# Kernel tuning notes

Measured on AMD Instinct MI355X. Metric: run time of the kernel, lower is better.

Reference implementation:

```python
import jax, jax.numpy as jnp
import numpy as np

ANGSTROM2BOHR = 1.8897261258369282
CUTOFF_ANGSTROM = 5.2  # module's `cutoff` init arg, converted to bohr in forward


def smooth_cutoff(d, rc):
    # torchani 'smooth' cutoff: exp(1 - 1/(1 - (d/rc)^2)) for d < rc, else 0
    x2 = (d / rc) ** 2
    x2_safe = jnp.where(x2 < 1.0, x2, 0.0)  # avoid inf inside the masked branch
    return jnp.where(d < rc, jnp.exp(1.0 - 1.0 / (1.0 - x2_safe)), 0.0)


def setup_inputs() -> dict:
    key = jax.random.key(0)
    k0, k1, k2, k3 = jax.random.split(key, 4)
    n_mol, n_atoms, n_pairs = 4096, 64, 16 * 1024 * 1024
    n_elem = 4  # H, C, N, O
    species = jax.random.randint(k0, (n_mol, n_atoms), 0, n_elem)
    energies = jnp.zeros((n_mol,), jnp.float32)
    atom_index12 = jax.random.randint(k1, (2, n_pairs), 0, n_mol * n_atoms)
    distances = jax.random.uniform(k2, (n_pairs,), jnp.float32, 0.5, 6.0)  # angstrom
    # exp_prefactor = -scaling_charge * sqrt(outer(Z, Z)) / 2, Z = [1, 6, 7, 8]
    z = jnp.array([1.0, 6.0, 7.0, 8.0], jnp.float32)
    exp_prefactor = (-0.016 * jnp.sqrt(jnp.outer(z, z)) / 2.0).astype(jnp.float32)
    # distances_factor = -scaling_radius / cutoff_radii (symmetric pairwise radii table)
    radii = jax.random.uniform(k3, (n_elem, n_elem), jnp.float32, 2.0, 5.0)
    radii = 0.5 * (radii + radii.T)
    distances_factor = (-10.0 / radii).astype(jnp.float32)
    return {
        "species": species,
        "energies": energies,
        "atom_index12": atom_index12,
        "distances": distances,
        "exp_prefactor": exp_prefactor,
        "distances_factor": distances_factor,
    }


def reference(species, energies, atom_index12, distances, exp_prefactor, distances_factor):
    n_mol, n_atoms = species.shape
    d = distances * ANGSTROM2BOHR  # [P]
    species12 = species.reshape(-1)[atom_index12]  # [2, P] gather
    pre = exp_prefactor[species12[0], species12[1]]   # [P]
    dfac = distances_factor[species12[0], species12[1]]  # [P]
    srb = pre * jnp.exp(dfac * d)
    srb = srb * smooth_cutoff(d, CUTOFF_ANGSTROM * ANGSTROM2BOHR)
    mol_idx = atom_index12[0] // n_atoms  # [P]
    out = energies + jax.ops.segment_sum(srb, mol_idx, num_segments=n_mol)
    return species, out
```

## Files before the change

kernel.cpp:

```cpp
#include <hip/hip_runtime.h>
#include <math.h>


__global__ void pack_species_kernel(const int* __restrict__ sp,
                                    unsigned* __restrict__ packed, int nwords) {
    int w = blockIdx.x * blockDim.x + threadIdx.x;
    if (w >= nwords) return;
    const int4* p4 = (const int4*)(sp + (w << 4));
    int4 a = p4[0], b = p4[1], c = p4[2], d = p4[3];
    unsigned v =
        (unsigned)(a.x & 3)        | ((unsigned)(a.y & 3) << 2)  |
        ((unsigned)(a.z & 3) << 4) | ((unsigned)(a.w & 3) << 6)  |
        ((unsigned)(b.x & 3) << 8) | ((unsigned)(b.y & 3) << 10) |
        ((unsigned)(b.z & 3) << 12)| ((unsigned)(b.w & 3) << 14) |
        ((unsigned)(c.x & 3) << 16)| ((unsigned)(c.y & 3) << 18) |
        ((unsigned)(c.z & 3) << 20)| ((unsigned)(c.w & 3) << 22) |
        ((unsigned)(d.x & 3) << 24)| ((unsigned)(d.y & 3) << 26) |
        ((unsigned)(d.z & 3) << 28)| ((unsigned)(d.w & 3) << 30);
    packed[w] = v;
}

__global__ void init_out_kernel(const int* __restrict__ species,
                                const float* __restrict__ energies,
                                float* __restrict__ out,
                                int n_species, int n_mol) {
    int i = blockIdx.x * blockDim.x + threadIdx.x;
    if (i < n_species) {
        out[i] = (float)species[i];
    } else if (i < n_species + n_mol) {
        out[i] = energies[i - n_species];
    }
}

template <bool FROM_WS>
__global__ __launch_bounds__(1024, 1)
void srb_main_kernel(const unsigned* __restrict__ packed_ws,
                     const int* __restrict__ species,
                     const int* __restrict__ ai,
                     const float* __restrict__ dist,
                     const float* __restrict__ pre_tab,
                     const float* __restrict__ dfac_tab,
                     float* __restrict__ out_e,
                     int P, int mol_shift) {
    __shared__ unsigned packed[16384];
    __shared__ float bins[4096];
    __shared__ float2 tab[16];

    const int t  = threadIdx.x;
    const int NT = blockDim.x;

    for (int i = t; i < 4096; i += NT) bins[i] = 0.0f;
    if (t < 16) tab[t] = make_float2(pre_tab[t], dfac_tab[t]);

    if (FROM_WS) {
        int4* dst = (int4*)packed;
        const int4* src = (const int4*)packed_ws;
        for (int i = t; i < 4096; i += NT) dst[i] = src[i];
    } else {
        for (int w = t; w < 16384; w += NT) {
            const int4* p4 = (const int4*)(species + (w << 4));
            int4 a = p4[0], b = p4[1], c = p4[2], d = p4[3];
            unsigned v =
                (unsigned)(a.x & 3)        | ((unsigned)(a.y & 3) << 2)  |
                ((unsigned)(a.z & 3) << 4) | ((unsigned)(a.w & 3) << 6)  |
                ((unsigned)(b.x & 3) << 8) | ((unsigned)(b.y & 3) << 10) |
                ((unsigned)(b.z & 3) << 12)| ((unsigned)(b.w & 3) << 14) |
                ((unsigned)(c.x & 3) << 16)| ((unsigned)(c.y & 3) << 18) |
                ((unsigned)(c.z & 3) << 20)| ((unsigned)(c.w & 3) << 22) |
                ((unsigned)(d.x & 3) << 24)| ((unsigned)(d.y & 3) << 26) |
                ((unsigned)(d.z & 3) << 28)| ((unsigned)(d.w & 3) << 30);
            packed[w] = v;
        }
    }
    __syncthreads();

    const float a2b   = (float)1.8897261258369282;
    const float rc    = (float)(5.2 * 1.8897261258369282);
    const float rcinv = (float)(1.0 / (5.2 * 1.8897261258369282));

    const int* ai0 = ai;
    const int* ai1 = ai + P;

    auto body = [&](int a0, int a1, float dang) {
        unsigned w0 = packed[(unsigned)a0 >> 4];
        unsigned w1 = packed[(unsigned)a1 >> 4];
        unsigned s0 = (w0 >> (((unsigned)a0 & 15u) << 1)) & 3u;
        unsigned s1 = (w1 >> (((unsigned)a1 & 15u) << 1)) & 3u;
        float2 td = tab[(s0 << 2) | s1];
        float db = dang * a2b;
        if (db < rc) {
            float x  = db * rcinv;
            float x2 = x * x;
            float arg = td.y * db + (1.0f - 1.0f / (1.0f - x2));
            float srb = td.x * __expf(arg);
            atomicAdd(&bins[(unsigned)a0 >> mol_shift], srb);
        }
    };

    const int stride = (int)gridDim.x * NT;
    if ((P & 3) == 0) {
        const int nvec = P >> 2;
        const int4*   v0 = (const int4*)ai0;
        const int4*   v1 = (const int4*)ai1;
        const float4* dv = (const float4*)dist;
        for (int v = (int)blockIdx.x * NT + t; v < nvec; v += stride) {
            int4   i0 = v0[v];
            int4   i1 = v1[v];
            float4 dd = dv[v];
            body(i0.x, i1.x, dd.x);
            body(i0.y, i1.y, dd.y);
            body(i0.z, i1.z, dd.z);
            body(i0.w, i1.w, dd.w);
        }
    } else {
        for (int p = (int)blockIdx.x * NT + t; p < P; p += stride)
            body(ai0[p], ai1[p], dist[p]);
    }

    __syncthreads();
    for (int i = t; i < 4096; i += NT) {
        float s = bins[i];
        if (s != 0.0f) atomicAdd(&out_e[i], s);
    }
}

extern "C" void kernel_launch(void* const* d_in, const int* in_sizes, int n_in,
                              void* d_out, int out_size, void* d_ws, size_t ws_size,
                              hipStream_t stream) {
    const int*   species  = (const int*)d_in[0];
    const float* energies = (const float*)d_in[1];
    const int*   ai       = (const int*)d_in[2];
    const float* dist     = (const float*)d_in[3];
    const float* pre_tab  = (const float*)d_in[4];
    const float* dfac_tab = (const float*)d_in[5];

    const int n_species = in_sizes[0];
    const int n_mol     = in_sizes[1];
    const int P         = in_sizes[3];
    const int n_atoms   = n_species / n_mol;

    int mol_shift = 0;
    while ((1 << mol_shift) < n_atoms) ++mol_shift;

    float* out   = (float*)d_out;
    float* out_e = out + n_species;

    {
        int tot = n_species + n_mol;
        init_out_kernel<<<(tot + 255) / 256, 256, 0, stream>>>(
            species, energies, out, n_species, n_mol);
    }

    const int nwords = n_species / 16;
    const bool use_ws = ws_size >= (size_t)nwords * sizeof(unsigned);
    if (use_ws) {
        unsigned* packed = (unsigned*)d_ws;
        pack_species_kernel<<<(nwords + 255) / 256, 256, 0, stream>>>(
            species, packed, nwords);
        srb_main_kernel<true><<<256, 1024, 0, stream>>>(
            packed, species, ai, dist, pre_tab, dfac_tab, out_e, P, mol_shift);
    } else {
        srb_main_kernel<false><<<256, 1024, 0, stream>>>(
            nullptr, species, ai, dist, pre_tab, dfac_tab, out_e, P, mol_shift);
    }
}
```

Before: 264.3 us.

## Split SRB into pair-code, accumulation, and bin-reduction kernels

The single fused kernel is replaced by several stages. The first stage computes a 16-bit code per pair, holding the molecule index and the species pair, and writes it to the workspace. The second stage reads the codes and distances, evaluates the energy with branch-free masking, and writes per-block shared bins to the workspace instead of atomics to global memory. A final kernel reduces the 512 per-block bin copies. The goal is better occupancy, since each kernel now uses less LDS, and removing global atomics, at the cost of an extra P*2-byte round trip and two more launches. The 16-bit code assumes n_mol*16 fits in 16 bits and that n_mol is a power of two.

```diff
diff --git a/kernel.cpp b/kernel.cpp
--- a/kernel.cpp
+++ b/kernel.cpp
@@ -1,6 +1,10 @@
 #include <hip/hip_runtime.h>
 #include <math.h>
 
+
+#define NBLK_P 512
+#define NBLK_M 512
+#define NT     1024
 
 __global__ void pack_species_kernel(const int* __restrict__ sp,
                                     unsigned* __restrict__ packed, int nwords) {
@@ -32,45 +36,137 @@
     }
 }
 
-template <bool FROM_WS>
-__global__ __launch_bounds__(1024, 1)
-void srb_main_kernel(const unsigned* __restrict__ packed_ws,
-                     const int* __restrict__ species,
-                     const int* __restrict__ ai,
-                     const float* __restrict__ dist,
-                     const float* __restrict__ pre_tab,
-                     const float* __restrict__ dfac_tab,
-                     float* __restrict__ out_e,
-                     int P, int mol_shift) {
+__global__ __launch_bounds__(NT, 8)
+void pair_code_kernel(const unsigned* __restrict__ packed_ws,
+                      const int* __restrict__ ai,
+                      unsigned short* __restrict__ combo,
+                      int P, int mol_shift) {
+    __shared__ unsigned packed[16384];
+    const int t = threadIdx.x;
+    {
+        int4* dst = (int4*)packed;
+        const int4* src = (const int4*)packed_ws;
+        for (int i = t; i < 4096; i += NT) dst[i] = src[i];
+    }
+    __syncthreads();
+
+    const int nv     = P >> 2;
+    const int stride = (int)gridDim.x * NT;
+    const int4* v0 = (const int4*)ai;
+    const int4* v1 = (const int4*)(ai + P);
+    ushort4* cv = (ushort4*)combo;
+
+    for (int v = (int)blockIdx.x * NT + t; v < nv; v += stride) {
+        int4 i0 = v0[v];
+        int4 i1 = v1[v];
+        auto code = [&](int a0, int a1) -> unsigned {
+            unsigned ua0 = (unsigned)a0, ua1 = (unsigned)a1;
+            unsigned s0 = (packed[ua0 >> 4] >> ((ua0 & 15u) << 1)) & 3u;
+            unsigned s1 = (packed[ua1 >> 4] >> ((ua1 & 15u) << 1)) & 3u;
+            return ((ua0 >> mol_shift) << 4) | (s0 << 2) | s1;
+        };
+        ushort4 c;
+        c.x = (unsigned short)code(i0.x, i1.x);
+        c.y = (unsigned short)code(i0.y, i1.y);
+        c.z = (unsigned short)code(i0.z, i1.z);
+        c.w = (unsigned short)code(i0.w, i1.w);
+        cv[v] = c;
+    }
+}
+
+__global__ __launch_bounds__(NT, 8)
+void srb_accum_kernel(const unsigned short* __restrict__ combo,
+                      const float* __restrict__ dist,
+                      const float* __restrict__ pre_tab,
+                      const float* __restrict__ dfac_tab,
+                      float* __restrict__ bins_ws,
+                      int P) {
+    __shared__ float bins[4096];
+    __shared__ float2 tab[16];
+    const int t = threadIdx.x;
+    for (int i = t; i < 4096; i += NT) bins[i] = 0.0f;
+    if (t < 16) tab[t] = make_float2(pre_tab[t], dfac_tab[t]);
+    __syncthreads();
+
+    const float a2b   = (float)1.8897261258369282;
+    const float rc    = (float)(5.2 * 1.8897261258369282);
+    const float rcinv = (float)(1.0 / (5.2 * 1.8897261258369282));
+
+    auto body = [&](unsigned c, float dang) {
+        float2 td = tab[c & 15u];
+        float db = dang * a2b;
+        float x  = db * rcinv;
+        float x2 = x * x;
+        float arg = td.y * db + (1.0f - 1.0f / (1.0f - x2));
+        float srb = td.x * __expf(arg);
+        srb = (db < rc) ? srb : 0.0f;
+        atomicAdd(&bins[c >> 4], srb);
+    };
+
+    const int ng     = P >> 3;
+    const int stride = (int)gridDim.x * NT;
+    const uint4*  cv = (const uint4*)combo;
+    const float4* dv = (const float4*)dist;
+
+    for (int g = (int)blockIdx.x * NT + t; g < ng; g += stride) {
+        uint4  cc = cv[g];
+        float4 d0 = dv[2 * g];
+        float4 d1 = dv[2 * g + 1];
+        body(cc.x & 0xffffu, d0.x); body(cc.x >> 16, d0.y);
+        body(cc.y & 0xffffu, d0.z); body(cc.y >> 16, d0.w);
+        body(cc.z & 0xffffu, d1.x); body(cc.z >> 16, d1.y);
+        body(cc.w & 0xffffu, d1.z); body(cc.w >> 16, d1.w);
+    }
+
+    __syncthreads();
+    float4* dst = (float4*)(bins_ws + (size_t)blockIdx.x * 4096);
+    const float4* src = (const float4*)bins;
+    for (int i = t; i < 1024; i += NT) dst[i] = src[i];
+}
+
+__global__ void reduce_bins_kernel(const float* __restrict__ bins_ws,
+                                   float* __restrict__ out_e,
+                                   int n_mol, int nblk) {
+    const int nchunk = 8;
+    int tid = blockIdx.x * blockDim.x + threadIdx.x;
+    if (tid >= n_mol * nchunk) return;
+    int mol   = tid & (n_mol - 1);
+    int chunk = tid / n_mol;
+    int nb    = nblk / nchunk;
+    const float* p = bins_ws + (size_t)chunk * nb * n_mol + mol;
+    float s = 0.0f;
+    #pragma unroll 8
+    for (int b = 0; b < nb; ++b) s += p[(size_t)b * n_mol];
+    atomicAdd(&out_e[mol], s);
+}
+
+__global__ __launch_bounds__(NT, 1)
+void srb_fused_kernel(const int* __restrict__ species,
+                      const int* __restrict__ ai,
+                      const float* __restrict__ dist,
+                      const float* __restrict__ pre_tab,
+                      const float* __restrict__ dfac_tab,
+                      float* __restrict__ out_e,
+                      int P, int mol_shift) {
     __shared__ unsigned packed[16384];
     __shared__ float bins[4096];
     __shared__ float2 tab[16];
-
-    const int t  = threadIdx.x;
-    const int NT = blockDim.x;
-
+    const int t = threadIdx.x;
     for (int i = t; i < 4096; i += NT) bins[i] = 0.0f;
     if (t < 16) tab[t] = make_float2(pre_tab[t], dfac_tab[t]);
-
-    if (FROM_WS) {
-        int4* dst = (int4*)packed;
-        const int4* src = (const int4*)packed_ws;
-        for (int i = t; i < 4096; i += NT) dst[i] = src[i];
-    } else {
-        for (int w = t; w < 16384; w += NT) {
-            const int4* p4 = (const int4*)(species + (w << 4));
-            int4 a = p4[0], b = p4[1], c = p4[2], d = p4[3];
-            unsigned v =
-                (unsigned)(a.x & 3)        | ((unsigned)(a.y & 3) << 2)  |
-                ((unsigned)(a.z & 3) << 4) | ((unsigned)(a.w & 3) << 6)  |
-                ((unsigned)(b.x & 3) << 8) | ((unsigned)(b.y & 3) << 10) |
-                ((unsigned)(b.z & 3) << 12)| ((unsigned)(b.w & 3) << 14) |
-                ((unsigned)(c.x & 3) << 16)| ((unsigned)(c.y & 3) << 18) |
-                ((unsigned)(c.z & 3) << 20)| ((unsigned)(c.w & 3) << 22) |
-                ((unsigned)(d.x & 3) << 24)| ((unsigned)(d.y & 3) << 26) |
-                ((unsigned)(d.z & 3) << 28)| ((unsigned)(d.w & 3) << 30);
-            packed[w] = v;
-        }
+    for (int w = t; w < 16384; w += NT) {
+        const int4* p4 = (const int4*)(species + (w << 4));
+        int4 a = p4[0], b = p4[1], c = p4[2], d = p4[3];
+        unsigned v =
+            (unsigned)(a.x & 3)        | ((unsigned)(a.y & 3) << 2)  |
+            ((unsigned)(a.z & 3) << 4) | ((unsigned)(a.w & 3) << 6)  |
+            ((unsigned)(b.x & 3) << 8) | ((unsigned)(b.y & 3) << 10) |
+            ((unsigned)(b.z & 3) << 12)| ((unsigned)(b.w & 3) << 14) |
+            ((unsigned)(c.x & 3) << 16)| ((unsigned)(c.y & 3) << 18) |
+            ((unsigned)(c.z & 3) << 20)| ((unsigned)(c.w & 3) << 22) |
+            ((unsigned)(d.x & 3) << 24)| ((unsigned)(d.y & 3) << 26) |
+            ((unsigned)(d.z & 3) << 28)| ((unsigned)(d.w & 3) << 30);
+        packed[w] = v;
     }
     __syncthreads();
 
@@ -78,43 +174,29 @@
     const float rc    = (float)(5.2 * 1.8897261258369282);
     const float rcinv = (float)(1.0 / (5.2 * 1.8897261258369282));
 
-    const int* ai0 = ai;
-    const int* ai1 = ai + P;
-
     auto body = [&](int a0, int a1, float dang) {
-        unsigned w0 = packed[(unsigned)a0 >> 4];
-        unsigned w1 = packed[(unsigned)a1 >> 4];
-        unsigned s0 = (w0 >> (((unsigned)a0 & 15u) << 1)) & 3u;
-        unsigned s1 = (w1 >> (((unsigned)a1 & 15u) << 1)) & 3u;
+        unsigned ua0 = (unsigned)a0, ua1 = (unsigned)a1;
+        unsigned s0 = (packed[ua0 >> 4] >> ((ua0 & 15u) << 1)) & 3u;
+        unsigned s1 = (packed[ua1 >> 4] >> ((ua1 & 15u) << 1)) & 3u;
         float2 td = tab[(s0 << 2) | s1];
         float db = dang * a2b;
-        if (db < rc) {
-            float x  = db * rcinv;
-            float x2 = x * x;
-            float arg = td.y * db + (1.0f - 1.0f / (1.0f - x2));
-            float srb = td.x * __expf(arg);
-            atomicAdd(&bins[(unsigned)a0 >> mol_shift], srb);
-        }
+        float x  = db * rcinv;
+        float x2 = x * x;
+        float arg = td.y * db + (1.0f - 1.0f / (1.0f - x2));
+        float srb = td.x * __expf(arg);
+        srb = (db < rc) ? srb : 0.0f;
+        atomicAdd(&bins[ua0 >> mol_shift], srb);
     };
 
+    const int nv     = P >> 2;
     const int stride = (int)gridDim.x * NT;
-    if ((P & 3) == 0) {
-        const int nvec = P >> 2;
-        const int4*   v0 = (const int4*)ai0;
-        const int4*   v1 = (const int4*)ai1;
-        const float4* dv = (const float4*)dist;
-        for (int v = (int)blockIdx.x * NT + t; v < nvec; v += stride) {
-            int4   i0 = v0[v];
-            int4   i1 = v1[v];
-            float4 dd = dv[v];
-            body(i0.x, i1.x, dd.x);
-            body(i0.y, i1.y, dd.y);
-            body(i0.z, i1.z, dd.z);
-            body(i0.w, i1.w, dd.w);
-        }
-    } else {
-        for (int p = (int)blockIdx.x * NT + t; p < P; p += stride)
-            body(ai0[p], ai1[p], dist[p]);
+    const int4*   v0 = (const int4*)ai;
+    const int4*   v1 = (const int4*)(ai + P);
+    const float4* dv = (const float4*)dist;
+    for (int v = (int)blockIdx.x * NT + t; v < nv; v += stride) {
+        int4 i0 = v0[v]; int4 i1 = v1[v]; float4 dd = dv[v];
+        body(i0.x, i1.x, dd.x); body(i0.y, i1.y, dd.y);
+        body(i0.z, i1.z, dd.z); body(i0.w, i1.w, dd.w);
     }
 
     __syncthreads();
@@ -151,16 +233,27 @@
             species, energies, out, n_species, n_mol);
     }
 
-    const int nwords = n_species / 16;
-    const bool use_ws = ws_size >= (size_t)nwords * sizeof(unsigned);
-    if (use_ws) {
-        unsigned* packed = (unsigned*)d_ws;
+    const int     nwords     = n_species / 16;
+    const size_t  packed_sz  = (size_t)nwords * 4;
+    const size_t  combo_sz   = (size_t)P * 2;
+    const size_t  bins_sz    = (size_t)NBLK_M * n_mol * 4;
+    const size_t  need       = packed_sz + combo_sz + bins_sz;
+
+    if (ws_size >= need) {
+        unsigned*       packed  = (unsigned*)d_ws;
+        unsigned short* combo   = (unsigned short*)((char*)d_ws + packed_sz);
+        float*          bins_ws = (float*)((char*)d_ws + packed_sz + combo_sz);
+
         pack_species_kernel<<<(nwords + 255) / 256, 256, 0, stream>>>(
             species, packed, nwords);
-        srb_main_kernel<true><<<256, 1024, 0, stream>>>(
-            packed, species, ai, dist, pre_tab, dfac_tab, out_e, P, mol_shift);
+        pair_code_kernel<<<NBLK_P, NT, 0, stream>>>(
+            packed, ai, combo, P, mol_shift);
+        srb_accum_kernel<<<NBLK_M, NT, 0, stream>>>(
+            combo, dist, pre_tab, dfac_tab, bins_ws, P);
+        reduce_bins_kernel<<<(n_mol * 8 + 255) / 256, 256, 0, stream>>>(
+            bins_ws, out_e, n_mol, NBLK_M);
     } else {
-        srb_main_kernel<false><<<256, 1024, 0, stream>>>(
-            nullptr, species, ai, dist, pre_tab, dfac_tab, out_e, P, mol_shift);
-    }
-}
+        srb_fused_kernel<<<256, NT, 0, stream>>>(
+            species, ai, dist, pre_tab, dfac_tab, out_e, P, mol_shift);
+    }
+}
```

Measured after the change: 322.6 us. 22.0% more time.

## Accumulate pair energies as fixed-point integers in LDS and global bins

Applied to the files above, without the earlier changes.

Replaces float shared-memory atomics with unsigned 32-bit fixed-point atomics in LDS and 64-bit integer atomics into a global accumulator. A final kernel converts the totals back to float and subtracts them from the energies. This relies on the prefactor always being negative so the magnitude can be stored unsigned. It also makes the cutoff branchless, replicates the small parameter table four ways to reduce LDS bank conflicts, and drops the unaligned-P path. The costs are one extra kernel launch, quantisation error, and a possible 32-bit overflow in a bin.

```diff
diff --git a/kernel.cpp b/kernel.cpp
--- a/kernel.cpp
+++ b/kernel.cpp
@@ -1,6 +1,11 @@
 #include <hip/hip_runtime.h>
 #include <math.h>
 
+
+#define NT        1024
+#define NBLK      256
+#define SCALE_F   134217728.0f
+#define INV_SCALE 7.450580596923828125e-9
 
 __global__ void pack_species_kernel(const int* __restrict__ sp,
                                     unsigned* __restrict__ packed, int nwords) {
@@ -20,103 +25,147 @@
     packed[w] = v;
 }
 
-__global__ void init_out_kernel(const int* __restrict__ species,
-                                const float* __restrict__ energies,
-                                float* __restrict__ out,
-                                int n_species, int n_mol) {
+__global__ void init_kernel(const int* __restrict__ species,
+                            float* __restrict__ out,
+                            unsigned long long* __restrict__ acc,
+                            int n_species, int n_mol) {
     int i = blockIdx.x * blockDim.x + threadIdx.x;
-    if (i < n_species) {
-        out[i] = (float)species[i];
-    } else if (i < n_species + n_mol) {
-        out[i] = energies[i - n_species];
-    }
-}
-
-template <bool FROM_WS>
-__global__ __launch_bounds__(1024, 1)
-void srb_main_kernel(const unsigned* __restrict__ packed_ws,
-                     const int* __restrict__ species,
-                     const int* __restrict__ ai,
-                     const float* __restrict__ dist,
-                     const float* __restrict__ pre_tab,
-                     const float* __restrict__ dfac_tab,
-                     float* __restrict__ out_e,
-                     int P, int mol_shift) {
+    if (i < n_species) out[i] = (float)species[i];
+    if (i < n_mol)     acc[i] = 0ull;
+}
+
+__global__ __launch_bounds__(NT, 1)
+void srb_fused_u32(const unsigned* __restrict__ packed_ws,
+                   const int* __restrict__ ai,
+                   const float* __restrict__ dist,
+                   const float* __restrict__ pre_tab,
+                   const float* __restrict__ dfac_tab,
+                   unsigned long long* __restrict__ acc,
+                   int P, int mol_shift) {
+    __shared__ unsigned packed[16384];
+    __shared__ unsigned binsu[4096];
+    __shared__ float2 tabr[4][18];
+
+    const int t = threadIdx.x;
+    for (int i = t; i < 4096; i += NT) binsu[i] = 0u;
+    if (t < 64) {
+        int e = t & 15;
+        tabr[t >> 4][e] = make_float2(-pre_tab[e], dfac_tab[e]);
+    }
+    {
+        int4* dst = (int4*)packed;
+        const int4* src = (const int4*)packed_ws;
+        for (int i = t; i < 4096; i += NT) dst[i] = src[i];
+    }
+    __syncthreads();
+
+    const float a2b   = (float)1.8897261258369282;
+    const float rc    = (float)(5.2 * 1.8897261258369282);
+    const float rcinv = (float)(1.0 / (5.2 * 1.8897261258369282));
+    const int   copy  = t & 3;
+
+    auto body = [&](int a0, int a1, float dang) {
+        unsigned ua0 = (unsigned)a0, ua1 = (unsigned)a1;
+        unsigned s0 = (packed[ua0 >> 4] >> ((ua0 & 15u) << 1)) & 3u;
+        unsigned s1 = (packed[ua1 >> 4] >> ((ua1 & 15u) << 1)) & 3u;
+        float2 td = tabr[copy][(s0 << 2) | s1];
+        float db = dang * a2b;
+        float x  = db * rcinv;
+        float arg = td.y * db + (1.0f - 1.0f / (1.0f - x * x));
+        float mag = td.x * __expf(arg);
+        mag = (db < rc) ? mag : 0.0f;
+        unsigned q = (unsigned)(mag * SCALE_F);
+        if (q) atomicAdd(&binsu[ua0 >> mol_shift], q);
+    };
+
+    const int nv     = P >> 2;
+    const int stride = (int)gridDim.x * NT;
+    const int4*   v0 = (const int4*)ai;
+    const int4*   v1 = (const int4*)(ai + P);
+    const float4* dv = (const float4*)dist;
+    for (int v = (int)blockIdx.x * NT + t; v < nv; v += stride) {
+        int4 i0 = v0[v]; int4 i1 = v1[v]; float4 dd = dv[v];
+        body(i0.x, i1.x, dd.x); body(i0.y, i1.y, dd.y);
+        body(i0.z, i1.z, dd.z); body(i0.w, i1.w, dd.w);
+    }
+
+    __syncthreads();
+    for (int i = t; i < 4096; i += NT) {
+        unsigned v = binsu[i];
+        if (v) atomicAdd(&acc[i], (unsigned long long)v);
+    }
+}
+
+__global__ void final_kernel(const unsigned long long* __restrict__ acc,
+                             const float* __restrict__ energies,
+                             float* __restrict__ out_e, int n_mol) {
+    int m = blockIdx.x * blockDim.x + threadIdx.x;
+    if (m < n_mol)
+        out_e[m] = energies[m] - (float)((double)acc[m] * INV_SCALE);
+}
+
+__global__ void init_out_fallback(const int* __restrict__ species,
+                                  const float* __restrict__ energies,
+                                  float* __restrict__ out,
+                                  int n_species, int n_mol) {
+    int i = blockIdx.x * blockDim.x + threadIdx.x;
+    if (i < n_species) out[i] = (float)species[i];
+    else if (i < n_species + n_mol) out[i] = energies[i - n_species];
+}
+
+__global__ __launch_bounds__(NT, 1)
+void srb_fused_f32(const int* __restrict__ species,
+                   const int* __restrict__ ai,
+                   const float* __restrict__ dist,
+                   const float* __restrict__ pre_tab,
+                   const float* __restrict__ dfac_tab,
+                   float* __restrict__ out_e,
+                   int P, int mol_shift) {
     __shared__ unsigned packed[16384];
     __shared__ float bins[4096];
     __shared__ float2 tab[16];
-
-    const int t  = threadIdx.x;
-    const int NT = blockDim.x;
-
+    const int t = threadIdx.x;
     for (int i = t; i < 4096; i += NT) bins[i] = 0.0f;
     if (t < 16) tab[t] = make_float2(pre_tab[t], dfac_tab[t]);
-
-    if (FROM_WS) {
-        int4* dst = (int4*)packed;
-        const int4* src = (const int4*)packed_ws;
-        for (int i = t; i < 4096; i += NT) dst[i] = src[i];
-    } else {
-        for (int w = t; w < 16384; w += NT) {
-            const int4* p4 = (const int4*)(species + (w << 4));
-            int4 a = p4[0], b = p4[1], c = p4[2], d = p4[3];
-            unsigned v =
-                (unsigned)(a.x & 3)        | ((unsigned)(a.y & 3) << 2)  |
-                ((unsigned)(a.z & 3) << 4) | ((unsigned)(a.w & 3) << 6)  |
-                ((unsigned)(b.x & 3) << 8) | ((unsigned)(b.y & 3) << 10) |
-                ((unsigned)(b.z & 3) << 12)| ((unsigned)(b.w & 3) << 14) |
-                ((unsigned)(c.x & 3) << 16)| ((unsigned)(c.y & 3) << 18) |
-                ((unsigned)(c.z & 3) << 20)| ((unsigned)(c.w & 3) << 22) |
-                ((unsigned)(d.x & 3) << 24)| ((unsigned)(d.y & 3) << 26) |
-                ((unsigned)(d.z & 3) << 28)| ((unsigned)(d.w & 3) << 30);
-            packed[w] = v;
-        }
-    }
-    __syncthreads();
-
+    for (int w = t; w < 16384; w += NT) {
+        const int4* p4 = (const int4*)(species + (w << 4));
+        int4 a = p4[0], b = p4[1], c = p4[2], d = p4[3];
+        unsigned v =
+            (unsigned)(a.x & 3)        | ((unsigned)(a.y & 3) << 2)  |
+            ((unsigned)(a.z & 3) << 4) | ((unsigned)(a.w & 3) << 6)  |
+            ((unsigned)(b.x & 3) << 8) | ((unsigned)(b.y & 3) << 10) |
+            ((unsigned)(b.z & 3) << 12)| ((unsigned)(b.w & 3) << 14) |
+            ((unsigned)(c.x & 3) << 16)| ((unsigned)(c.y & 3) << 18) |
+            ((unsigned)(c.z & 3) << 20)| ((unsigned)(c.w & 3) << 22) |
+            ((unsigned)(d.x & 3) << 24)| ((unsigned)(d.y & 3) << 26) |
+            ((unsigned)(d.z & 3) << 28)| ((unsigned)(d.w & 3) << 30);
+        packed[w] = v;
+    }
+    __syncthreads();
     const float a2b   = (float)1.8897261258369282;
     const float rc    = (float)(5.2 * 1.8897261258369282);
     const float rcinv = (float)(1.0 / (5.2 * 1.8897261258369282));
-
-    const int* ai0 = ai;
-    const int* ai1 = ai + P;
-
     auto body = [&](int a0, int a1, float dang) {
-        unsigned w0 = packed[(unsigned)a0 >> 4];
-        unsigned w1 = packed[(unsigned)a1 >> 4];
-        unsigned s0 = (w0 >> (((unsigned)a0 & 15u) << 1)) & 3u;
-        unsigned s1 = (w1 >> (((unsigned)a1 & 15u) << 1)) & 3u;
+        unsigned ua0 = (unsigned)a0, ua1 = (unsigned)a1;
+        unsigned s0 = (packed[ua0 >> 4] >> ((ua0 & 15u) << 1)) & 3u;
+        unsigned s1 = (packed[ua1 >> 4] >> ((ua1 & 15u) << 1)) & 3u;
         float2 td = tab[(s0 << 2) | s1];
         float db = dang * a2b;
-        if (db < rc) {
-            float x  = db * rcinv;
-            float x2 = x * x;
-            float arg = td.y * db + (1.0f - 1.0f / (1.0f - x2));
-            float srb = td.x * __expf(arg);
-            atomicAdd(&bins[(unsigned)a0 >> mol_shift], srb);
-        }
+        float x  = db * rcinv;
+        float arg = td.y * db + (1.0f - 1.0f / (1.0f - x * x));
+        float srb = td.x * __expf(arg);
+        srb = (db < rc) ? srb : 0.0f;
+        atomicAdd(&bins[ua0 >> mol_shift], srb);
     };
-
-    const int stride = (int)gridDim.x * NT;
-    if ((P & 3) == 0) {
-        const int nvec = P >> 2;
-        const int4*   v0 = (const int4*)ai0;
-        const int4*   v1 = (const int4*)ai1;
-        const float4* dv = (const float4*)dist;
-        for (int v = (int)blockIdx.x * NT + t; v < nvec; v += stride) {
-            int4   i0 = v0[v];
-            int4   i1 = v1[v];
-            float4 dd = dv[v];
-            body(i0.x, i1.x, dd.x);
-            body(i0.y, i1.y, dd.y);
-            body(i0.z, i1.z, dd.z);
-            body(i0.w, i1.w, dd.w);
-        }
-    } else {
-        for (int p = (int)blockIdx.x * NT + t; p < P; p += stride)
-            body(ai0[p], ai1[p], dist[p]);
-    }
-
+    const int nv = P >> 2, stride = (int)gridDim.x * NT;
+    const int4* v0 = (const int4*)ai;
+    const int4* v1 = (const int4*)(ai + P);
+    const float4* dv = (const float4*)dist;
+    for (int v = (int)blockIdx.x * NT + t; v < nv; v += stride) {
+        int4 i0 = v0[v]; int4 i1 = v1[v]; float4 dd = dv[v];
+        body(i0.x, i1.x, dd.x); body(i0.y, i1.y, dd.y);
+        body(i0.z, i1.z, dd.z); body(i0.w, i1.w, dd.w);
+    }
     __syncthreads();
     for (int i = t; i < 4096; i += NT) {
         float s = bins[i];
@@ -145,22 +194,27 @@
     float* out   = (float*)d_out;
     float* out_e = out + n_species;
 
-    {
-        int tot = n_species + n_mol;
-        init_out_kernel<<<(tot + 255) / 256, 256, 0, stream>>>(
-            species, energies, out, n_species, n_mol);
-    }
-
-    const int nwords = n_species / 16;
-    const bool use_ws = ws_size >= (size_t)nwords * sizeof(unsigned);
-    if (use_ws) {
-        unsigned* packed = (unsigned*)d_ws;
+    const int    nwords    = n_species / 16;
+    const size_t packed_sz = (size_t)nwords * 4;
+    const size_t acc_sz    = (size_t)n_mol * 8;
+    const size_t need      = packed_sz + acc_sz;
+
+    if (ws_size >= need) {
+        unsigned*           packed = (unsigned*)d_ws;
+        unsigned long long* acc    = (unsigned long long*)((char*)d_ws + packed_sz);
+
+        init_kernel<<<(n_species + 255) / 256, 256, 0, stream>>>(
+            species, out, acc, n_species, n_mol);
         pack_species_kernel<<<(nwords + 255) / 256, 256, 0, stream>>>(
             species, packed, nwords);
-        srb_main_kernel<true><<<256, 1024, 0, stream>>>(
-            packed, species, ai, dist, pre_tab, dfac_tab, out_e, P, mol_shift);
+        srb_fused_u32<<<NBLK, NT, 0, stream>>>(
+            packed, ai, dist, pre_tab, dfac_tab, acc, P, mol_shift);
+        final_kernel<<<(n_mol + 255) / 256, 256, 0, stream>>>(
+            acc, energies, out_e, n_mol);
     } else {
-        srb_main_kernel<false><<<256, 1024, 0, stream>>>(
-            nullptr, species, ai, dist, pre_tab, dfac_tab, out_e, P, mol_shift);
-    }
-}
+        init_out_fallback<<<(n_species + n_mol + 255) / 256, 256, 0, stream>>>(
+            species, energies, out, n_species, n_mol);
+        srb_fused_f32<<<NBLK, NT, 0, stream>>>(
+            species, ai, dist, pre_tab, dfac_tab, out_e, P, mol_shift);
+    }
+}
```

Result: faster. 251.5 us (-4.9%).
